# Kernel optimization log

Measured on AMD Instinct MI355X. Metric: run time of the kernel, lower is better.

## Reference

```python
import jax, jax.numpy as jnp
import numpy as np

B, S, HID, NH = 2, 2048, 1024, 16
HD = HID // NH

def setup_inputs() -> dict:
    key = jax.random.key(0)
    ks = jax.random.split(key, 9)
    s = 1.0 / np.sqrt(HID)
    return {
        "hidden_state": jax.random.normal(ks[0], (B, S, HID), jnp.float32),
        "Wq": jax.random.normal(ks[1], (HID, HID), jnp.float32) * s,
        "bq": jax.random.normal(ks[2], (HID,), jnp.float32) * 0.02,
        "Wk": jax.random.normal(ks[3], (HID, HID), jnp.float32) * s,
        "bk": jax.random.normal(ks[4], (HID,), jnp.float32) * 0.02,
        "Wv": jax.random.normal(ks[5], (HID, HID), jnp.float32) * s,
        "bv": jax.random.normal(ks[6], (HID,), jnp.float32) * 0.02,
        "Wo": jax.random.normal(ks[7], (HID, HID), jnp.float32) * s,
        "bo": jax.random.normal(ks[8], (HID,), jnp.float32) * 0.02,
    }

def _split_heads(x):
    # [B,S,HID] -> [B,NH,S,HD]
    b, s, _ = x.shape
    return x.reshape(b, s, NH, HD).transpose(0, 2, 1, 3)

def reference(hidden_state, Wq, bq, Wk, bk, Wv, bv, Wo, bo):
    # torch nn.Linear: y = x @ W.T + b
    q = _split_heads(hidden_state @ Wq.T + bq)
    k = _split_heads(hidden_state @ Wk.T + bk)
    v = _split_heads(hidden_state @ Wv.T + bv)
    scale = 1.0 / jnp.sqrt(jnp.asarray(HD, hidden_state.dtype))
    scores = jnp.einsum("bhqd,bhkd->bhqk", q, k) * scale
    probs = jax.nn.softmax(scores, axis=-1)
    out = jnp.einsum("bhqk,bhkd->bhqd", probs, v)  # [B,NH,S,HD]
    out = out.transpose(0, 2, 1, 3).reshape(hidden_state.shape[0], -1, NH * HD)
    return out @ Wo.T + bo
```

## Files before the change

### kernel.cpp

```cpp
#include <hip/hip_runtime.h>


#define S_LEN 2048
#define HID   1024
#define NHEAD 16
#define HDIM  64
#define M_TOT 4096
#define LOG2E 1.4426950408889634f

typedef __attribute__((ext_vector_type(8))) short bf16x8;
typedef __attribute__((ext_vector_type(4))) float f32x4;

static __device__ __forceinline__ float b2f(short s) {
  union { unsigned int u; float f; } v;
  v.u = ((unsigned int)(unsigned short)s) << 16;
  return v.f;
}
static __device__ __forceinline__ short f2b(float f) {
  union { unsigned int u; float f; } v; v.f = f;
  unsigned int r = (v.u + 0x7FFFu + ((v.u >> 16) & 1u)) >> 16;
  return (short)(unsigned short)r;
}
static __device__ __forceinline__ short f2b_fast(float f) {
  union { unsigned int u; float f; } v; v.f = f;
  return (short)(unsigned short)((v.u + 0x8000u) >> 16);
}
static __device__ __forceinline__ float fexp2(float x) { return exp2f(x); }

#define GLD_LDS16(g, l)                                                        \
  __builtin_amdgcn_global_load_lds(                                            \
      (const __attribute__((address_space(1))) void*)(g),                      \
      (__attribute__((address_space(3))) void*)(l), 16, 0, 0)

__global__ __launch_bounds__(256) void detect_kernel(
    const unsigned short* __restrict__ X16, int* __restrict__ flag)
{
  __shared__ int cnt;
  if (threadIdx.x == 0) cnt = 0;
  __syncthreads();
  int local = 0;
  for (int i = threadIdx.x; i < 16384; i += 256) {
    unsigned short u = X16[i];
    int e = (u >> 7) & 0xFF;
    if (u == 0 || (e >= 0x60 && e <= 0x9F)) local++;
  }
  atomicAdd(&cnt, local);
  __syncthreads();
  if (threadIdx.x == 0) *flag = (cnt < 15000) ? 1 : 0;
}

__global__ __launch_bounds__(256) void convert_all_kernel(
    const void* s0, const void* s1, const void* s2, const void* s3,
    const void* s4, const void* s5, const void* s6, const void* s7,
    const void* s8,
    short* d0, short* d1, short* d2, short* d3, short* d4,
    short* d5, short* d6, short* d7, short* d8,
    const int* __restrict__ flagp)
{
  const void* src; short* dst; int n;
  switch (blockIdx.y) {
    case 0: src = s0; dst = d0; n = M_TOT * HID; break;
    case 1: src = s1; dst = d1; n = HID * HID; break;
    case 2: src = s2; dst = d2; n = HID; break;
    case 3: src = s3; dst = d3; n = HID * HID; break;
    case 4: src = s4; dst = d4; n = HID; break;
    case 5: src = s5; dst = d5; n = HID * HID; break;
    case 6: src = s6; dst = d6; n = HID; break;
    case 7: src = s7; dst = d7; n = HID * HID; break;
    default: src = s8; dst = d8; n = HID; break;
  }
  const int f = *flagp;
  const long stride = (long)gridDim.x * 256 * 4;
  long i = ((long)blockIdx.x * 256 + threadIdx.x) * 4;
  if (f) {
    const float* sf = (const float*)src;
    for (; i < n; i += stride) {
      float4 v = *(const float4*)(sf + i);
      ushort4 o;
      o.x = (unsigned short)f2b(v.x); o.y = (unsigned short)f2b(v.y);
      o.z = (unsigned short)f2b(v.z); o.w = (unsigned short)f2b(v.w);
      *(ushort4*)(dst + i) = o;
    }
  } else {
    const short* ss = (const short*)src;
    for (; i < n; i += stride)
      *(uint2*)(dst + i) = *(const uint2*)(ss + i);
  }
}

static __device__ __forceinline__ void gemm_core_128x128(
    const short* __restrict__ A, const short* __restrict__ W,
    int bm, int n0, short* Alds, short* Wlds, f32x4 acc[4][4])
{
  const int t    = threadIdx.x;
  const int lane = t & 63;
  const int w    = t >> 6;
  const int wm   = w >> 1, wn = w & 1;
  const int quad = lane >> 4, l15 = lane & 15;

  const int srow = t >> 3;
  const int cg   = (t & 7) ^ (srow & 7);
  const short* Ag = A + (size_t)(bm + srow) * HID + cg * 8;
  const short* Wg = W + (size_t)(n0 + srow) * HID + cg * 8;

  for (int k0 = 0; k0 < HID; k0 += 64) {
    __syncthreads();
#pragma unroll
    for (int i = 0; i < 4; ++i) {
      GLD_LDS16(Ag + (size_t)i * 32 * HID + k0, Alds + i * 2048 + t * 8);
      GLD_LDS16(Wg + (size_t)i * 32 * HID + k0, Wlds + i * 2048 + t * 8);
    }
    __syncthreads();

    bf16x8 af[4][2], bfr[4][2];
#pragma unroll
    for (int mt = 0; mt < 4; ++mt)
#pragma unroll
      for (int ks = 0; ks < 2; ++ks)
        af[mt][ks] = *(const bf16x8*)(Alds + (wm * 64 + mt * 16 + l15) * 64 +
                                      (((ks * 4 + quad) ^ (l15 & 7)) * 8));
#pragma unroll
    for (int nt = 0; nt < 4; ++nt)
#pragma unroll
      for (int ks = 0; ks < 2; ++ks)
        bfr[nt][ks] = *(const bf16x8*)(Wlds + (wn * 64 + nt * 16 + l15) * 64 +
                                       (((ks * 4 + quad) ^ (l15 & 7)) * 8));
#pragma unroll
    for (int mt = 0; mt < 4; ++mt)
#pragma unroll
      for (int nt = 0; nt < 4; ++nt) {
        acc[mt][nt] = __builtin_amdgcn_mfma_f32_16x16x32_bf16(af[mt][0], bfr[nt][0], acc[mt][nt], 0, 0, 0);
        acc[mt][nt] = __builtin_amdgcn_mfma_f32_16x16x32_bf16(af[mt][1], bfr[nt][1], acc[mt][nt], 0, 0, 0);
      }
  }
}

__global__ __launch_bounds__(256) void gemm_qkv_kernel(
    const short* __restrict__ X,
    const short* __restrict__ Wq, const short* __restrict__ Wk, const short* __restrict__ Wv,
    const short* __restrict__ bq, const short* __restrict__ bk, const short* __restrict__ bv,
    short* __restrict__ Q, short* __restrict__ K, short* __restrict__ V)
{
  __shared__ short Alds[128 * 64];
  __shared__ short Wlds[128 * 64];
  const int which = blockIdx.y >> 3;
  const int n0    = (blockIdx.y & 7) * 128;
  const int bm    = blockIdx.x * 128;
  const short* W    = (which == 0) ? Wq : (which == 1) ? Wk : Wv;
  const short* bias = (which == 0) ? bq : (which == 1) ? bk : bv;

  f32x4 acc[4][4];
#pragma unroll
  for (int i = 0; i < 4; ++i)
#pragma unroll
    for (int j = 0; j < 4; ++j) acc[i][j] = (f32x4){0.f, 0.f, 0.f, 0.f};

  gemm_core_128x128(X, W, bm, n0, Alds, Wlds, acc);

  const int t = threadIdx.x, lane = t & 63, w = t >> 6;
  const int wm = w >> 1, wn = w & 1;
  const int quad = lane >> 4, l15 = lane & 15;
  const float qscale = 0.125f * LOG2E;
#pragma unroll
  for (int nt = 0; nt < 4; ++nt) {
    const int n = n0 + wn * 64 + nt * 16 + l15;
    const float bvv = b2f(bias[n]);
#pragma unroll
    for (int mt = 0; mt < 4; ++mt) {
#pragma unroll
      for (int r = 0; r < 4; ++r) {
        const int m = bm + wm * 64 + mt * 16 + quad * 4 + r;
        const float val = acc[mt][nt][r] + bvv;
        if (which == 0) {
          Q[(size_t)m * HID + n] = f2b(val * qscale);
        } else if (which == 1) {
          K[(size_t)m * HID + n] = f2b(val);
        } else {
          const int b = m >> 11, s = m & 2047;
          V[((size_t)(b * 1024 + n)) * 2048 + s] = f2b(val);
        }
      }
    }
  }
}

static __device__ __forceinline__ void gemm_core_128x64(
    const short* __restrict__ A, const short* __restrict__ W,
    int bm, int n0, short* Alds, short* Wlds, f32x4 acc[2][4])
{
  const int t    = threadIdx.x;
  const int lane = t & 63;
  const int w    = t >> 6;
  const int quad = lane >> 4, l15 = lane & 15;

  const int srow = t >> 3;
  const int cg   = (t & 7) ^ (srow & 7);
  const short* Ag = A + (size_t)(bm + srow) * HID + cg * 8;
  const short* Wg = W + (size_t)(n0 + srow) * HID + cg * 8;

  for (int k0 = 0; k0 < HID; k0 += 64) {
    __syncthreads();
#pragma unroll
    for (int i = 0; i < 4; ++i)
      GLD_LDS16(Ag + (size_t)i * 32 * HID + k0, Alds + i * 2048 + t * 8);
#pragma unroll
    for (int i = 0; i < 2; ++i)
      GLD_LDS16(Wg + (size_t)i * 32 * HID + k0, Wlds + i * 2048 + t * 8);
    __syncthreads();

    bf16x8 af[2][2], bfr[4][2];
#pragma unroll
    for (int mt = 0; mt < 2; ++mt)
#pragma unroll
      for (int ks = 0; ks < 2; ++ks)
        af[mt][ks] = *(const bf16x8*)(Alds + (w * 32 + mt * 16 + l15) * 64 +
                                      (((ks * 4 + quad) ^ (l15 & 7)) * 8));
#pragma unroll
    for (int nt = 0; nt < 4; ++nt)
#pragma unroll
      for (int ks = 0; ks < 2; ++ks)
        bfr[nt][ks] = *(const bf16x8*)(Wlds + (nt * 16 + l15) * 64 +
                                       (((ks * 4 + quad) ^ (l15 & 7)) * 8));
#pragma unroll
    for (int mt = 0; mt < 2; ++mt)
#pragma unroll
      for (int nt = 0; nt < 4; ++nt) {
        acc[mt][nt] = __builtin_amdgcn_mfma_f32_16x16x32_bf16(af[mt][0], bfr[nt][0], acc[mt][nt], 0, 0, 0);
        acc[mt][nt] = __builtin_amdgcn_mfma_f32_16x16x32_bf16(af[mt][1], bfr[nt][1], acc[mt][nt], 0, 0, 0);
      }
  }
}

__global__ __launch_bounds__(256) void gemm_o_kernel(
    const short* __restrict__ A, const short* __restrict__ W,
    const short* __restrict__ bias, void* __restrict__ out,
    const int* __restrict__ flagp)
{
  __shared__ short Alds[128 * 64];
  __shared__ short Wlds[64 * 64];
  const int n0 = blockIdx.y * 64;
  const int bm = blockIdx.x * 128;
  const int f32out = *flagp;

  f32x4 acc[2][4];
#pragma unroll
  for (int i = 0; i < 2; ++i)
#pragma unroll
    for (int j = 0; j < 4; ++j) acc[i][j] = (f32x4){0.f, 0.f, 0.f, 0.f};

  gemm_core_128x64(A, W, bm, n0, Alds, Wlds, acc);

  const int t = threadIdx.x, lane = t & 63, w = t >> 6;
  const int quad = lane >> 4, l15 = lane & 15;
#pragma unroll
  for (int nt = 0; nt < 4; ++nt) {
    const int n = n0 + nt * 16 + l15;
    const float bvv = b2f(bias[n]);
#pragma unroll
    for (int mt = 0; mt < 2; ++mt) {
#pragma unroll
      for (int r = 0; r < 4; ++r) {
        const int m = bm + w * 32 + mt * 16 + quad * 4 + r;
        const float val = acc[mt][nt][r] + bvv;
        const size_t idx = (size_t)m * HID + n;
        if (f32out) ((float*)out)[idx] = val;
        else        ((short*)out)[idx] = f2b(val);
      }
    }
  }
}

__global__ __launch_bounds__(256) void flash_attn_kernel(
    const short* __restrict__ Q, const short* __restrict__ K,
    const short* __restrict__ V, short* __restrict__ O)
{
  __shared__ short Kl0[64 * 64], Kl1[64 * 64];
  __shared__ short Vl0[64 * 64], Vl1[64 * 64];
  __shared__ short Pl[4 * 32 * 64];

  const int t    = threadIdx.x;
  const int lane = t & 63, w = t >> 6;
  const int quad = lane >> 4, l15 = lane & 15;
  const int qtile = blockIdx.x;
  const int bh    = blockIdx.y;
  const int b = bh >> 4, h = bh & 15;
  const int hoff = h * HDIM;

  bf16x8 qf[2][2];
#pragma unroll
  for (int mt = 0; mt < 2; ++mt) {
    const int qrow = b * S_LEN + qtile * 128 + w * 32 + mt * 16 + l15;
#pragma unroll
    for (int ks = 0; ks < 2; ++ks)
      qf[mt][ks] = *(const bf16x8*)(Q + (size_t)qrow * HID + hoff + ks * 32 + quad * 8);
  }

  f32x4 o[2][4], ol[2];
#pragma unroll
  for (int mt = 0; mt < 2; ++mt) {
#pragma unroll
    for (int nt = 0; nt < 4; ++nt) o[mt][nt] = (f32x4){0.f, 0.f, 0.f, 0.f};
    ol[mt] = (f32x4){0.f, 0.f, 0.f, 0.f};
  }

  bf16x8 vones;
#pragma unroll
  for (int j = 0; j < 8; ++j) vones[j] = (short)0x3F80;

  short* myP = Pl + w * (32 * 64);
  const int srow = t >> 3;
  const int cg   = (t & 7) ^ (srow & 7);
  const short* Kg = K + (size_t)(b * S_LEN) * HID + hoff + cg * 8;
  const short* Vg = V + (size_t)(bh * HDIM) * S_LEN + cg * 8;

  auto stage = [&](short* dK, short* dV, int kv0) {
    GLD_LDS16(Kg + (size_t)(kv0 + srow) * HID,      dK + t * 8);
    GLD_LDS16(Kg + (size_t)(kv0 + 32 + srow) * HID, dK + 2048 + t * 8);
    GLD_LDS16(Vg + (size_t)srow * S_LEN + kv0,        dV + t * 8);
    GLD_LDS16(Vg + (size_t)(32 + srow) * S_LEN + kv0, dV + 2048 + t * 8);
  };

  auto step = [&](int it, const short* Kc, const short* Vc, short* Kn, short* Vn) {
    __syncthreads();
    if (it < 31) stage(Kn, Vn, (it + 1) * 64);

    bf16x8 kf[4][2];
#pragma unroll
    for (int kt = 0; kt < 4; ++kt)
#pragma unroll
      for (int ks = 0; ks < 2; ++ks)
        kf[kt][ks] = *(const bf16x8*)(Kc + (kt * 16 + l15) * 64 +
                                      (((ks * 4 + quad) ^ (l15 & 7)) * 8));

#pragma unroll
    for (int mt = 0; mt < 2; ++mt) {
      f32x4 s[4];
#pragma unroll
      for (int kt = 0; kt < 4; ++kt) {
        s[kt] = (f32x4){0.f, 0.f, 0.f, 0.f};
        s[kt] = __builtin_amdgcn_mfma_f32_16x16x32_bf16(qf[mt][0], kf[kt][0], s[kt], 0, 0, 0);
        s[kt] = __builtin_amdgcn_mfma_f32_16x16x32_bf16(qf[mt][1], kf[kt][1], s[kt], 0, 0, 0);
      }
      short* Pm = myP + mt * (16 * 64);
#pragma unroll
      for (int kt = 0; kt < 4; ++kt)
#pragma unroll
        for (int r = 0; r < 4; ++r)
          Pm[(quad * 4 + r) * 64 + (((kt * 2 + (l15 >> 3)) ^ quad) * 8) + (l15 & 7)] =
              f2b_fast(fexp2(s[kt][r]));
    }

    bf16x8 pa[2][2];
#pragma unroll
    for (int mt = 0; mt < 2; ++mt)
#pragma unroll
      for (int ks = 0; ks < 2; ++ks)
        pa[mt][ks] = *(const bf16x8*)(myP + (mt * 16 + l15) * 64 +
                                      (((ks * 4 + quad) ^ ((l15 >> 2) & 3)) * 8));

#pragma unroll
    for (int nt = 0; nt < 4; ++nt) {
#pragma unroll
      for (int ks = 0; ks < 2; ++ks) {
        bf16x8 vf = *(const bf16x8*)(Vc + (nt * 16 + l15) * 64 +
                                     (((ks * 4 + quad) ^ (l15 & 7)) * 8));
        o[0][nt] = __builtin_amdgcn_mfma_f32_16x16x32_bf16(pa[0][ks], vf, o[0][nt], 0, 0, 0);
        o[1][nt] = __builtin_amdgcn_mfma_f32_16x16x32_bf16(pa[1][ks], vf, o[1][nt], 0, 0, 0);
      }
    }
#pragma unroll
    for (int mt = 0; mt < 2; ++mt) {
      ol[mt] = __builtin_amdgcn_mfma_f32_16x16x32_bf16(pa[mt][0], vones, ol[mt], 0, 0, 0);
      ol[mt] = __builtin_amdgcn_mfma_f32_16x16x32_bf16(pa[mt][1], vones, ol[mt], 0, 0, 0);
    }
  };

  stage(Kl0, Vl0, 0);
#pragma unroll 1
  for (int it = 0; it < 32; it += 2) {
    step(it,     Kl0, Vl0, Kl1, Vl1);
    step(it + 1, Kl1, Vl1, Kl0, Vl0);
  }

#pragma unroll
  for (int mt = 0; mt < 2; ++mt) {
    const int orow = b * S_LEN + qtile * 128 + w * 32 + mt * 16 + quad * 4;
#pragma unroll
    for (int nt = 0; nt < 4; ++nt) {
      const int col = hoff + nt * 16 + l15;
#pragma unroll
      for (int r = 0; r < 4; ++r)
        O[(size_t)(orow + r) * HID + col] = f2b(o[mt][nt][r] / ol[mt][r]);
    }
  }
}

extern "C" void kernel_launch(void* const* d_in, const int* in_sizes, int n_in,
                              void* d_out, int out_size, void* d_ws, size_t ws_size,
                              hipStream_t stream) {
  short* WS  = (short*)d_ws;
  const size_t M1 = 1024 * 1024;
  short* Xc  = WS;
  short* Wqc = WS + 4 * M1;
  short* Wkc = WS + 5 * M1;
  short* Wvc = WS + 6 * M1;
  short* Woc = WS + 7 * M1;
  short* bqc = WS + 8 * M1;
  short* bkc = bqc + 1024;
  short* bvc = bkc + 1024;
  short* boc = bvc + 1024;
  short* Qb  = WS + 9 * M1;
  short* Kb  = WS + 13 * M1;
  short* Vt  = WS + 17 * M1;
  short* An  = WS + 21 * M1;
  int*   flag = (int*)(WS + 25 * M1);

  detect_kernel<<<1, 256, 0, stream>>>((const unsigned short*)d_in[0], flag);

  convert_all_kernel<<<dim3(128, 9), 256, 0, stream>>>(
      d_in[0], d_in[1], d_in[2], d_in[3], d_in[4], d_in[5], d_in[6], d_in[7], d_in[8],
      Xc, Wqc, bqc, Wkc, bkc, Wvc, bvc, Woc, boc, flag);

  gemm_qkv_kernel<<<dim3(32, 24), 256, 0, stream>>>(
      Xc, Wqc, Wkc, Wvc, bqc, bkc, bvc, Qb, Kb, Vt);

  flash_attn_kernel<<<dim3(16, 32), 256, 0, stream>>>(Qb, Kb, Vt, An);

  gemm_o_kernel<<<dim3(32, 16), 256, 0, stream>>>(An, Woc, boc, d_out, flag);
}
```

Baseline: 237.5 us.

## Split attention KV range across waves with LDS reduction, direct global K/V loads

Restructures the attention kernel so each block handles 64 query rows and each of the four waves processes a quarter of the key sequence. K and V fragments are loaded directly from global memory into registers, dropping the LDS staging and per-step barriers. Partial outputs and row sums are combined through shared memory at the end. The grid doubles to raise parallelism, at the cost of more register pressure, uncoalesced global loads, and a final cross-wave reduction. Also switches exp2 to the hardware builtin.

```diff
diff --git a/kernel.cpp b/kernel.cpp
--- a/kernel.cpp
+++ b/kernel.cpp
@@ -25,7 +25,13 @@
   union { unsigned int u; float f; } v; v.f = f;
   return (short)(unsigned short)((v.u + 0x8000u) >> 16);
 }
-static __device__ __forceinline__ float fexp2(float x) { return exp2f(x); }
+static __device__ __forceinline__ float fexp2(float x) {
+#if __has_builtin(__builtin_amdgcn_exp2f)
+  return __builtin_amdgcn_exp2f(x);
+#else
+  return exp2f(x);
+#endif
+}
 
 #define GLD_LDS16(g, l)                                                        \
   __builtin_amdgcn_global_load_lds(                                            \
@@ -274,9 +280,7 @@
     const short* __restrict__ Q, const short* __restrict__ K,
     const short* __restrict__ V, short* __restrict__ O)
 {
-  __shared__ short Kl0[64 * 64], Kl1[64 * 64];
-  __shared__ short Vl0[64 * 64], Vl1[64 * 64];
-  __shared__ short Pl[4 * 32 * 64];
+  __shared__ __align__(16) unsigned char smem[49920];
 
   const int t    = threadIdx.x;
   const int lane = t & 63, w = t >> 6;
@@ -286,18 +290,18 @@
   const int b = bh >> 4, h = bh & 15;
   const int hoff = h * HDIM;
 
-  bf16x8 qf[2][2];
-#pragma unroll
-  for (int mt = 0; mt < 2; ++mt) {
-    const int qrow = b * S_LEN + qtile * 128 + w * 32 + mt * 16 + l15;
+  bf16x8 qf[4][2];
+#pragma unroll
+  for (int mt = 0; mt < 4; ++mt) {
+    const int qrow = b * S_LEN + qtile * 64 + mt * 16 + l15;
 #pragma unroll
     for (int ks = 0; ks < 2; ++ks)
       qf[mt][ks] = *(const bf16x8*)(Q + (size_t)qrow * HID + hoff + ks * 32 + quad * 8);
   }
 
-  f32x4 o[2][4], ol[2];
-#pragma unroll
-  for (int mt = 0; mt < 2; ++mt) {
+  f32x4 o[4][4], ol[4];
+#pragma unroll
+  for (int mt = 0; mt < 4; ++mt) {
 #pragma unroll
     for (int nt = 0; nt < 4; ++nt) o[mt][nt] = (f32x4){0.f, 0.f, 0.f, 0.f};
     ol[mt] = (f32x4){0.f, 0.f, 0.f, 0.f};
@@ -307,52 +311,46 @@
 #pragma unroll
   for (int j = 0; j < 8; ++j) vones[j] = (short)0x3F80;
 
-  short* myP = Pl + w * (32 * 64);
-  const int srow = t >> 3;
-  const int cg   = (t & 7) ^ (srow & 7);
-  const short* Kg = K + (size_t)(b * S_LEN) * HID + hoff + cg * 8;
-  const short* Vg = V + (size_t)(bh * HDIM) * S_LEN + cg * 8;
-
-  auto stage = [&](short* dK, short* dV, int kv0) {
-    GLD_LDS16(Kg + (size_t)(kv0 + srow) * HID,      dK + t * 8);
-    GLD_LDS16(Kg + (size_t)(kv0 + 32 + srow) * HID, dK + 2048 + t * 8);
-    GLD_LDS16(Vg + (size_t)srow * S_LEN + kv0,        dV + t * 8);
-    GLD_LDS16(Vg + (size_t)(32 + srow) * S_LEN + kv0, dV + 2048 + t * 8);
-  };
-
-  auto step = [&](int it, const short* Kc, const short* Vc, short* Kn, short* Vn) {
-    __syncthreads();
-    if (it < 31) stage(Kn, Vn, (it + 1) * 64);
+  short* myP = (short*)smem + w * 4096;
+  const short* Kg = K + (size_t)(b * S_LEN + l15) * HID + hoff + quad * 8;
+  const short* Vg = V + (size_t)(bh * HDIM + l15) * S_LEN + quad * 8;
+
+#pragma unroll 1
+  for (int it = 0; it < 8; ++it) {
+    const int kv0 = w * 512 + it * 64;
 
     bf16x8 kf[4][2];
 #pragma unroll
     for (int kt = 0; kt < 4; ++kt)
 #pragma unroll
       for (int ks = 0; ks < 2; ++ks)
-        kf[kt][ks] = *(const bf16x8*)(Kc + (kt * 16 + l15) * 64 +
-                                      (((ks * 4 + quad) ^ (l15 & 7)) * 8));
-
-#pragma unroll
-    for (int mt = 0; mt < 2; ++mt) {
-      f32x4 s[4];
+        kf[kt][ks] = *(const bf16x8*)(Kg + (size_t)(kv0 + kt * 16) * HID + ks * 32);
+
+    f32x4 s[4][4];
+#pragma unroll
+    for (int mt = 0; mt < 4; ++mt)
 #pragma unroll
       for (int kt = 0; kt < 4; ++kt) {
-        s[kt] = (f32x4){0.f, 0.f, 0.f, 0.f};
-        s[kt] = __builtin_amdgcn_mfma_f32_16x16x32_bf16(qf[mt][0], kf[kt][0], s[kt], 0, 0, 0);
-        s[kt] = __builtin_amdgcn_mfma_f32_16x16x32_bf16(qf[mt][1], kf[kt][1], s[kt], 0, 0, 0);
-      }
+        f32x4 acc = (f32x4){0.f, 0.f, 0.f, 0.f};
+        acc = __builtin_amdgcn_mfma_f32_16x16x32_bf16(qf[mt][0], kf[kt][0], acc, 0, 0, 0);
+        acc = __builtin_amdgcn_mfma_f32_16x16x32_bf16(qf[mt][1], kf[kt][1], acc, 0, 0, 0);
+        s[mt][kt] = acc;
+      }
+
+#pragma unroll
+    for (int mt = 0; mt < 4; ++mt) {
       short* Pm = myP + mt * (16 * 64);
 #pragma unroll
       for (int kt = 0; kt < 4; ++kt)
 #pragma unroll
         for (int r = 0; r < 4; ++r)
           Pm[(quad * 4 + r) * 64 + (((kt * 2 + (l15 >> 3)) ^ quad) * 8) + (l15 & 7)] =
-              f2b_fast(fexp2(s[kt][r]));
-    }
-
-    bf16x8 pa[2][2];
-#pragma unroll
-    for (int mt = 0; mt < 2; ++mt)
+              f2b_fast(fexp2(s[mt][kt][r]));
+    }
+
+    bf16x8 pa[4][2];
+#pragma unroll
+    for (int mt = 0; mt < 4; ++mt)
 #pragma unroll
       for (int ks = 0; ks < 2; ++ks)
         pa[mt][ks] = *(const bf16x8*)(myP + (mt * 16 + l15) * 64 +
@@ -362,35 +360,63 @@
     for (int nt = 0; nt < 4; ++nt) {
 #pragma unroll
       for (int ks = 0; ks < 2; ++ks) {
-        bf16x8 vf = *(const bf16x8*)(Vc + (nt * 16 + l15) * 64 +
-                                     (((ks * 4 + quad) ^ (l15 & 7)) * 8));
-        o[0][nt] = __builtin_amdgcn_mfma_f32_16x16x32_bf16(pa[0][ks], vf, o[0][nt], 0, 0, 0);
-        o[1][nt] = __builtin_amdgcn_mfma_f32_16x16x32_bf16(pa[1][ks], vf, o[1][nt], 0, 0, 0);
-      }
-    }
-#pragma unroll
-    for (int mt = 0; mt < 2; ++mt) {
+        bf16x8 vf = *(const bf16x8*)(Vg + (size_t)(nt * 16) * S_LEN + kv0 + ks * 32);
+#pragma unroll
+        for (int mt = 0; mt < 4; ++mt)
+          o[mt][nt] = __builtin_amdgcn_mfma_f32_16x16x32_bf16(pa[mt][ks], vf, o[mt][nt], 0, 0, 0);
+      }
+    }
+#pragma unroll
+    for (int mt = 0; mt < 4; ++mt) {
       ol[mt] = __builtin_amdgcn_mfma_f32_16x16x32_bf16(pa[mt][0], vones, ol[mt], 0, 0, 0);
       ol[mt] = __builtin_amdgcn_mfma_f32_16x16x32_bf16(pa[mt][1], vones, ol[mt], 0, 0, 0);
     }
-  };
-
-  stage(Kl0, Vl0, 0);
-#pragma unroll 1
-  for (int it = 0; it < 32; it += 2) {
-    step(it,     Kl0, Vl0, Kl1, Vl1);
-    step(it + 1, Kl1, Vl1, Kl0, Vl0);
-  }
-
-#pragma unroll
-  for (int mt = 0; mt < 2; ++mt) {
-    const int orow = b * S_LEN + qtile * 128 + w * 32 + mt * 16 + quad * 4;
-#pragma unroll
-    for (int nt = 0; nt < 4; ++nt) {
-      const int col = hoff + nt * 16 + l15;
-#pragma unroll
-      for (int r = 0; r < 4; ++r)
-        O[(size_t)(orow + r) * HID + col] = f2b(o[mt][nt][r] / ol[mt][r]);
+  }
+
+  __syncthreads();
+  float* Osh  = (float*)smem;
+  float* OLsh = (float*)(smem + 49152);
+  if (w > 0) {
+#pragma unroll
+    for (int mt = 0; mt < 4; ++mt)
+#pragma unroll
+      for (int nt = 0; nt < 4; ++nt)
+#pragma unroll
+        for (int r = 0; r < 4; ++r)
+          Osh[(w - 1) * 4096 + (mt * 16 + quad * 4 + r) * 64 + nt * 16 + l15] = o[mt][nt][r];
+    if (l15 == 0) {
+#pragma unroll
+      for (int mt = 0; mt < 4; ++mt)
+#pragma unroll
+        for (int r = 0; r < 4; ++r)
+          OLsh[(w - 1) * 64 + mt * 16 + quad * 4 + r] = ol[mt][r];
+    }
+  }
+  __syncthreads();
+  if (w == 0) {
+#pragma unroll
+    for (int wj = 0; wj < 3; ++wj)
+#pragma unroll
+      for (int mt = 0; mt < 4; ++mt) {
+#pragma unroll
+        for (int nt = 0; nt < 4; ++nt)
+#pragma unroll
+          for (int r = 0; r < 4; ++r)
+            o[mt][nt][r] += Osh[wj * 4096 + (mt * 16 + quad * 4 + r) * 64 + nt * 16 + l15];
+#pragma unroll
+        for (int r = 0; r < 4; ++r)
+          ol[mt][r] += OLsh[wj * 64 + mt * 16 + quad * 4 + r];
+      }
+#pragma unroll
+    for (int mt = 0; mt < 4; ++mt) {
+      const int orow = b * S_LEN + qtile * 64 + mt * 16 + quad * 4;
+#pragma unroll
+      for (int nt = 0; nt < 4; ++nt) {
+        const int col = hoff + nt * 16 + l15;
+#pragma unroll
+        for (int r = 0; r < 4; ++r)
+          O[(size_t)(orow + r) * HID + col] = f2b(o[mt][nt][r] / ol[mt][r]);
+      }
     }
   }
 }
@@ -424,7 +450,7 @@
   gemm_qkv_kernel<<<dim3(32, 24), 256, 0, stream>>>(
       Xc, Wqc, Wkc, Wvc, bqc, bkc, bvc, Qb, Kb, Vt);
 
-  flash_attn_kernel<<<dim3(16, 32), 256, 0, stream>>>(Qb, Kb, Vt, An);
+  flash_attn_kernel<<<dim3(32, 32), 256, 0, stream>>>(Qb, Kb, Vt, An);
 
   gemm_o_kernel<<<dim3(32, 16), 256, 0, stream>>>(An, Woc, boc, d_out, flag);
 }
```

Measured after the change: 285.7 us. +20.3%, slower.

## Drop dtype detection, shrink QKV tiles to 128x64, stage V transpose via LDS

Applied to the files above, without the earlier changes.

Removes the detect kernel and the runtime dtype flag, so inputs are always converted from fp32 and the output is written as fp32. The QKV GEMM moves from 128x128 to 128x64 tiles, doubling the grid to 1536 blocks for better CU occupancy. The transposed V store now goes through LDS and is written out as contiguous 16-byte vectors instead of scattered 2-byte stores. The smaller tiles reduce operand reuse per block, which raises global and LDS traffic per FLOP.

```diff
diff --git a/kernel.cpp b/kernel.cpp
--- a/kernel.cpp
+++ b/kernel.cpp
@@ -32,32 +32,14 @@
       (const __attribute__((address_space(1))) void*)(g),                      \
       (__attribute__((address_space(3))) void*)(l), 16, 0, 0)
 
-__global__ __launch_bounds__(256) void detect_kernel(
-    const unsigned short* __restrict__ X16, int* __restrict__ flag)
+__global__ __launch_bounds__(256) void convert_all_kernel(
+    const float* s0, const float* s1, const float* s2, const float* s3,
+    const float* s4, const float* s5, const float* s6, const float* s7,
+    const float* s8,
+    short* d0, short* d1, short* d2, short* d3, short* d4,
+    short* d5, short* d6, short* d7, short* d8)
 {
-  __shared__ int cnt;
-  if (threadIdx.x == 0) cnt = 0;
-  __syncthreads();
-  int local = 0;
-  for (int i = threadIdx.x; i < 16384; i += 256) {
-    unsigned short u = X16[i];
-    int e = (u >> 7) & 0xFF;
-    if (u == 0 || (e >= 0x60 && e <= 0x9F)) local++;
-  }
-  atomicAdd(&cnt, local);
-  __syncthreads();
-  if (threadIdx.x == 0) *flag = (cnt < 15000) ? 1 : 0;
-}
-
-__global__ __launch_bounds__(256) void convert_all_kernel(
-    const void* s0, const void* s1, const void* s2, const void* s3,
-    const void* s4, const void* s5, const void* s6, const void* s7,
-    const void* s8,
-    short* d0, short* d1, short* d2, short* d3, short* d4,
-    short* d5, short* d6, short* d7, short* d8,
-    const int* __restrict__ flagp)
-{
-  const void* src; short* dst; int n;
+  const float* src; short* dst; int n;
   switch (blockIdx.y) {
     case 0: src = s0; dst = d0; n = M_TOT * HID; break;
     case 1: src = s1; dst = d1; n = HID * HID; break;
@@ -69,69 +51,14 @@
     case 7: src = s7; dst = d7; n = HID * HID; break;
     default: src = s8; dst = d8; n = HID; break;
   }
-  const int f = *flagp;
-  const long stride = (long)gridDim.x * 256 * 4;
-  long i = ((long)blockIdx.x * 256 + threadIdx.x) * 4;
-  if (f) {
-    const float* sf = (const float*)src;
-    for (; i < n; i += stride) {
-      float4 v = *(const float4*)(sf + i);
-      ushort4 o;
-      o.x = (unsigned short)f2b(v.x); o.y = (unsigned short)f2b(v.y);
-      o.z = (unsigned short)f2b(v.z); o.w = (unsigned short)f2b(v.w);
-      *(ushort4*)(dst + i) = o;
-    }
-  } else {
-    const short* ss = (const short*)src;
-    for (; i < n; i += stride)
-      *(uint2*)(dst + i) = *(const uint2*)(ss + i);
-  }
-}
-
-static __device__ __forceinline__ void gemm_core_128x128(
-    const short* __restrict__ A, const short* __restrict__ W,
-    int bm, int n0, short* Alds, short* Wlds, f32x4 acc[4][4])
-{
-  const int t    = threadIdx.x;
-  const int lane = t & 63;
-  const int w    = t >> 6;
-  const int wm   = w >> 1, wn = w & 1;
-  const int quad = lane >> 4, l15 = lane & 15;
-
-  const int srow = t >> 3;
-  const int cg   = (t & 7) ^ (srow & 7);
-  const short* Ag = A + (size_t)(bm + srow) * HID + cg * 8;
-  const short* Wg = W + (size_t)(n0 + srow) * HID + cg * 8;
-
-  for (int k0 = 0; k0 < HID; k0 += 64) {
-    __syncthreads();
-#pragma unroll
-    for (int i = 0; i < 4; ++i) {
-      GLD_LDS16(Ag + (size_t)i * 32 * HID + k0, Alds + i * 2048 + t * 8);
-      GLD_LDS16(Wg + (size_t)i * 32 * HID + k0, Wlds + i * 2048 + t * 8);
-    }
-    __syncthreads();
-
-    bf16x8 af[4][2], bfr[4][2];
-#pragma unroll
-    for (int mt = 0; mt < 4; ++mt)
-#pragma unroll
-      for (int ks = 0; ks < 2; ++ks)
-        af[mt][ks] = *(const bf16x8*)(Alds + (wm * 64 + mt * 16 + l15) * 64 +
-                                      (((ks * 4 + quad) ^ (l15 & 7)) * 8));
-#pragma unroll
-    for (int nt = 0; nt < 4; ++nt)
-#pragma unroll
-      for (int ks = 0; ks < 2; ++ks)
-        bfr[nt][ks] = *(const bf16x8*)(Wlds + (wn * 64 + nt * 16 + l15) * 64 +
-                                       (((ks * 4 + quad) ^ (l15 & 7)) * 8));
-#pragma unroll
-    for (int mt = 0; mt < 4; ++mt)
-#pragma unroll
-      for (int nt = 0; nt < 4; ++nt) {
-        acc[mt][nt] = __builtin_amdgcn_mfma_f32_16x16x32_bf16(af[mt][0], bfr[nt][0], acc[mt][nt], 0, 0, 0);
-        acc[mt][nt] = __builtin_amdgcn_mfma_f32_16x16x32_bf16(af[mt][1], bfr[nt][1], acc[mt][nt], 0, 0, 0);
-      }
+  const int stride = gridDim.x * 256 * 4;
+  int i = (blockIdx.x * 256 + threadIdx.x) * 4;
+  for (; i < n; i += stride) {
+    float4 v = *(const float4*)(src + i);
+    ushort4 o;
+    o.x = (unsigned short)f2b(v.x); o.y = (unsigned short)f2b(v.y);
+    o.z = (unsigned short)f2b(v.z); o.w = (unsigned short)f2b(v.w);
+    *(ushort4*)(dst + i) = o;
   }
 }
 
@@ -141,106 +68,122 @@
     const short* __restrict__ bq, const short* __restrict__ bk, const short* __restrict__ bv,
     short* __restrict__ Q, short* __restrict__ K, short* __restrict__ V)
 {
-  __shared__ short Alds[128 * 64];
-  __shared__ short Wlds[128 * 64];
-  const int which = blockIdx.y >> 3;
-  const int n0    = (blockIdx.y & 7) * 128;
+  __shared__ short Alds[8704];
+  __shared__ short Wlds[64 * 64];
+  const int ntile = blockIdx.y;
+  const int which = ntile >> 4;
+  const int n0    = (ntile & 15) * 64;
   const int bm    = blockIdx.x * 128;
   const short* W    = (which == 0) ? Wq : (which == 1) ? Wk : Wv;
   const short* bias = (which == 0) ? bq : (which == 1) ? bk : bv;
 
-  f32x4 acc[4][4];
-#pragma unroll
-  for (int i = 0; i < 4; ++i)
-#pragma unroll
-    for (int j = 0; j < 4; ++j) acc[i][j] = (f32x4){0.f, 0.f, 0.f, 0.f};
-
-  gemm_core_128x128(X, W, bm, n0, Alds, Wlds, acc);
-
-  const int t = threadIdx.x, lane = t & 63, w = t >> 6;
-  const int wm = w >> 1, wn = w & 1;
-  const int quad = lane >> 4, l15 = lane & 15;
-  const float qscale = 0.125f * LOG2E;
-#pragma unroll
-  for (int nt = 0; nt < 4; ++nt) {
-    const int n = n0 + wn * 64 + nt * 16 + l15;
-    const float bvv = b2f(bias[n]);
-#pragma unroll
-    for (int mt = 0; mt < 4; ++mt) {
-#pragma unroll
-      for (int r = 0; r < 4; ++r) {
-        const int m = bm + wm * 64 + mt * 16 + quad * 4 + r;
-        const float val = acc[mt][nt][r] + bvv;
-        if (which == 0) {
-          Q[(size_t)m * HID + n] = f2b(val * qscale);
-        } else if (which == 1) {
-          K[(size_t)m * HID + n] = f2b(val);
-        } else {
-          const int b = m >> 11, s = m & 2047;
-          V[((size_t)(b * 1024 + n)) * 2048 + s] = f2b(val);
-        }
-      }
-    }
-  }
-}
-
-static __device__ __forceinline__ void gemm_core_128x64(
-    const short* __restrict__ A, const short* __restrict__ W,
-    int bm, int n0, short* Alds, short* Wlds, f32x4 acc[2][4])
-{
   const int t    = threadIdx.x;
   const int lane = t & 63;
   const int w    = t >> 6;
   const int quad = lane >> 4, l15 = lane & 15;
 
-  const int srow = t >> 3;
-  const int cg   = (t & 7) ^ (srow & 7);
-  const short* Ag = A + (size_t)(bm + srow) * HID + cg * 8;
-  const short* Wg = W + (size_t)(n0 + srow) * HID + cg * 8;
-
-  for (int k0 = 0; k0 < HID; k0 += 64) {
+  f32x4 acc[2][4];
+#pragma unroll
+  for (int i = 0; i < 2; ++i)
+#pragma unroll
+    for (int j = 0; j < 4; ++j) acc[i][j] = (f32x4){0.f, 0.f, 0.f, 0.f};
+
+  {
+    const int srow = t >> 3;
+    const int cg   = (t & 7) ^ (srow & 7);
+    const short* Ag = X + (size_t)(bm + srow) * HID + cg * 8;
+    const short* Wg = W + (size_t)(n0 + srow) * HID + cg * 8;
+
+    for (int k0 = 0; k0 < HID; k0 += 64) {
+      __syncthreads();
+#pragma unroll
+      for (int i = 0; i < 4; ++i)
+        GLD_LDS16(Ag + (size_t)i * 32 * HID + k0, Alds + i * 2048 + t * 8);
+#pragma unroll
+      for (int i = 0; i < 2; ++i)
+        GLD_LDS16(Wg + (size_t)i * 32 * HID + k0, Wlds + i * 2048 + t * 8);
+      __syncthreads();
+
+      bf16x8 af[2][2], bfr[4][2];
+#pragma unroll
+      for (int mt = 0; mt < 2; ++mt)
+#pragma unroll
+        for (int ks = 0; ks < 2; ++ks)
+          af[mt][ks] = *(const bf16x8*)(Alds + (w * 32 + mt * 16 + l15) * 64 +
+                                        (((ks * 4 + quad) ^ (l15 & 7)) * 8));
+#pragma unroll
+      for (int nt = 0; nt < 4; ++nt)
+#pragma unroll
+        for (int ks = 0; ks < 2; ++ks)
+          bfr[nt][ks] = *(const bf16x8*)(Wlds + (nt * 16 + l15) * 64 +
+                                         (((ks * 4 + quad) ^ (l15 & 7)) * 8));
+#pragma unroll
+      for (int mt = 0; mt < 2; ++mt)
+#pragma unroll
+        for (int nt = 0; nt < 4; ++nt) {
+          acc[mt][nt] = __builtin_amdgcn_mfma_f32_16x16x32_bf16(af[mt][0], bfr[nt][0], acc[mt][nt], 0, 0, 0);
+          acc[mt][nt] = __builtin_amdgcn_mfma_f32_16x16x32_bf16(af[mt][1], bfr[nt][1], acc[mt][nt], 0, 0, 0);
+        }
+    }
+  }
+
+  if (which != 2) {
+    short* Out = (which == 0) ? Q : K;
+    const float scl = (which == 0) ? 0.125f * LOG2E : 1.0f;
+#pragma unroll
+    for (int nt = 0; nt < 4; ++nt) {
+      const int n = n0 + nt * 16 + l15;
+      const float bvv = b2f(bias[n]);
+#pragma unroll
+      for (int mt = 0; mt < 2; ++mt)
+#pragma unroll
+        for (int r = 0; r < 4; ++r) {
+          const int m = bm + w * 32 + mt * 16 + quad * 4 + r;
+          Out[(size_t)m * HID + n] = f2b((acc[mt][nt][r] + bvv) * scl);
+        }
+    }
+  } else {
     __syncthreads();
 #pragma unroll
-    for (int i = 0; i < 4; ++i)
-      GLD_LDS16(Ag + (size_t)i * 32 * HID + k0, Alds + i * 2048 + t * 8);
-#pragma unroll
-    for (int i = 0; i < 2; ++i)
-      GLD_LDS16(Wg + (size_t)i * 32 * HID + k0, Wlds + i * 2048 + t * 8);
+    for (int nt = 0; nt < 4; ++nt) {
+      const int n = nt * 16 + l15;
+      const float bvv = b2f(bias[n0 + n]);
+#pragma unroll
+      for (int mt = 0; mt < 2; ++mt) {
+        const int m = w * 32 + mt * 16 + quad * 4;
+#pragma unroll
+        for (int r = 0; r < 4; r += 2) {
+          union { unsigned int u; short s2[2]; } pk;
+          pk.s2[0] = f2b(acc[mt][nt][r] + bvv);
+          pk.s2[1] = f2b(acc[mt][nt][r + 1] + bvv);
+          *(unsigned int*)(Alds + n * 136 + m + r) = pk.u;
+        }
+      }
+    }
     __syncthreads();
-
-    bf16x8 af[2][2], bfr[4][2];
-#pragma unroll
-    for (int mt = 0; mt < 2; ++mt)
-#pragma unroll
-      for (int ks = 0; ks < 2; ++ks)
-        af[mt][ks] = *(const bf16x8*)(Alds + (w * 32 + mt * 16 + l15) * 64 +
-                                      (((ks * 4 + quad) ^ (l15 & 7)) * 8));
-#pragma unroll
-    for (int nt = 0; nt < 4; ++nt)
-#pragma unroll
-      for (int ks = 0; ks < 2; ++ks)
-        bfr[nt][ks] = *(const bf16x8*)(Wlds + (nt * 16 + l15) * 64 +
-                                       (((ks * 4 + quad) ^ (l15 & 7)) * 8));
-#pragma unroll
-    for (int mt = 0; mt < 2; ++mt)
-#pragma unroll
-      for (int nt = 0; nt < 4; ++nt) {
-        acc[mt][nt] = __builtin_amdgcn_mfma_f32_16x16x32_bf16(af[mt][0], bfr[nt][0], acc[mt][nt], 0, 0, 0);
-        acc[mt][nt] = __builtin_amdgcn_mfma_f32_16x16x32_bf16(af[mt][1], bfr[nt][1], acc[mt][nt], 0, 0, 0);
-      }
+    const int nr   = t >> 2;
+    const int mseg = (t & 3) * 32;
+    const int bb = bm >> 11, s0 = bm & 2047;
+    short* dst = V + ((size_t)(bb * 1024 + n0 + nr)) * 2048 + s0 + mseg;
+#pragma unroll
+    for (int k = 0; k < 4; ++k)
+      *(bf16x8*)(dst + k * 8) = *(const bf16x8*)(Alds + nr * 136 + mseg + k * 8);
   }
 }
 
 __global__ __launch_bounds__(256) void gemm_o_kernel(
     const short* __restrict__ A, const short* __restrict__ W,
-    const short* __restrict__ bias, void* __restrict__ out,
-    const int* __restrict__ flagp)
+    const short* __restrict__ bias, float* __restrict__ out)
 {
   __shared__ short Alds[128 * 64];
   __shared__ short Wlds[64 * 64];
   const int n0 = blockIdx.y * 64;
   const int bm = blockIdx.x * 128;
-  const int f32out = *flagp;
+
+  const int t    = threadIdx.x;
+  const int lane = t & 63;
+  const int w    = t >> 6;
+  const int quad = lane >> 4, l15 = lane & 15;
 
   f32x4 acc[2][4];
 #pragma unroll
@@ -248,25 +191,54 @@
 #pragma unroll
     for (int j = 0; j < 4; ++j) acc[i][j] = (f32x4){0.f, 0.f, 0.f, 0.f};
 
-  gemm_core_128x64(A, W, bm, n0, Alds, Wlds, acc);
-
-  const int t = threadIdx.x, lane = t & 63, w = t >> 6;
-  const int quad = lane >> 4, l15 = lane & 15;
+  const int srow = t >> 3;
+  const int cg   = (t & 7) ^ (srow & 7);
+  const short* Ag = A + (size_t)(bm + srow) * HID + cg * 8;
+  const short* Wg = W + (size_t)(n0 + srow) * HID + cg * 8;
+
+  for (int k0 = 0; k0 < HID; k0 += 64) {
+    __syncthreads();
+#pragma unroll
+    for (int i = 0; i < 4; ++i)
+      GLD_LDS16(Ag + (size_t)i * 32 * HID + k0, Alds + i * 2048 + t * 8);
+#pragma unroll
+    for (int i = 0; i < 2; ++i)
+      GLD_LDS16(Wg + (size_t)i * 32 * HID + k0, Wlds + i * 2048 + t * 8);
+    __syncthreads();
+
+    bf16x8 af[2][2], bfr[4][2];
+#pragma unroll
+    for (int mt = 0; mt < 2; ++mt)
+#pragma unroll
+      for (int ks = 0; ks < 2; ++ks)
+        af[mt][ks] = *(const bf16x8*)(Alds + (w * 32 + mt * 16 + l15) * 64 +
+                                      (((ks * 4 + quad) ^ (l15 & 7)) * 8));
+#pragma unroll
+    for (int nt = 0; nt < 4; ++nt)
+#pragma unroll
+      for (int ks = 0; ks < 2; ++ks)
+        bfr[nt][ks] = *(const bf16x8*)(Wlds + (nt * 16 + l15) * 64 +
+                                       (((ks * 4 + quad) ^ (l15 & 7)) * 8));
+#pragma unroll
+    for (int mt = 0; mt < 2; ++mt)
+#pragma unroll
+      for (int nt = 0; nt < 4; ++nt) {
+        acc[mt][nt] = __builtin_amdgcn_mfma_f32_16x16x32_bf16(af[mt][0], bfr[nt][0], acc[mt][nt], 0, 0, 0);
+        acc[mt][nt] = __builtin_amdgcn_mfma_f32_16x16x32_bf16(af[mt][1], bfr[nt][1], acc[mt][nt], 0, 0, 0);
+      }
+  }
+
 #pragma unroll
   for (int nt = 0; nt < 4; ++nt) {
     const int n = n0 + nt * 16 + l15;
     const float bvv = b2f(bias[n]);
 #pragma unroll
-    for (int mt = 0; mt < 2; ++mt) {
+    for (int mt = 0; mt < 2; ++mt)
 #pragma unroll
       for (int r = 0; r < 4; ++r) {
         const int m = bm + w * 32 + mt * 16 + quad * 4 + r;
-        const float val = acc[mt][nt][r] + bvv;
-        const size_t idx = (size_t)m * HID + n;
-        if (f32out) ((float*)out)[idx] = val;
-        else        ((short*)out)[idx] = f2b(val);
+        out[(size_t)m * HID + n] = acc[mt][nt][r] + bvv;
       }
-    }
   }
 }
 
@@ -413,18 +385,17 @@
   short* Kb  = WS + 13 * M1;
   short* Vt  = WS + 17 * M1;
   short* An  = WS + 21 * M1;
-  int*   flag = (int*)(WS + 25 * M1);
-
-  detect_kernel<<<1, 256, 0, stream>>>((const unsigned short*)d_in[0], flag);
 
   convert_all_kernel<<<dim3(128, 9), 256, 0, stream>>>(
-      d_in[0], d_in[1], d_in[2], d_in[3], d_in[4], d_in[5], d_in[6], d_in[7], d_in[8],
-      Xc, Wqc, bqc, Wkc, bkc, Wvc, bvc, Woc, boc, flag);
-
-  gemm_qkv_kernel<<<dim3(32, 24), 256, 0, stream>>>(
+      (const float*)d_in[0], (const float*)d_in[1], (const float*)d_in[2],
+      (const float*)d_in[3], (const float*)d_in[4], (const float*)d_in[5],
+      (const float*)d_in[6], (const float*)d_in[7], (const float*)d_in[8],
+      Xc, Wqc, bqc, Wkc, bkc, Wvc, bvc, Woc, boc);
+
+  gemm_qkv_kernel<<<dim3(32, 48), 256, 0, stream>>>(
       Xc, Wqc, Wkc, Wvc, bqc, bkc, bvc, Qb, Kb, Vt);
 
   flash_attn_kernel<<<dim3(16, 32), 256, 0, stream>>>(Qb, Kb, Vt, An);
 
-  gemm_o_kernel<<<dim3(32, 16), 256, 0, stream>>>(An, Woc, boc, d_out, flag);
-}
+  gemm_o_kernel<<<dim3(32, 16), 256, 0, stream>>>(An, Woc, boc, (float*)d_out);
+}
```

Result: faster. 220.4 us (-7.2%).
